# Kernel optimization log

Measured on AMD Instinct MI355X. Metric: run time of the kernel, lower is better.

Reference implementation:

```python
import jax, jax.numpy as jnp
import numpy as np

B, H, L, C, KD, NS = 4, 1024, 8192, 1, 64, 8  # batch, d_model, seq_len, channels, kernel_dim, num_scales
DECAY_MIN, DECAY_MAX = 1.0, 4.0


def _interp_linear(x, scale):
    """F.interpolate(mode='linear', align_corners=False) for integer scale on last axis."""
    if scale == 1:
        return x
    Lin = x.shape[-1]
    Lout = Lin * scale
    pos = (jnp.arange(Lout, dtype=x.dtype) + 0.5) / scale - 0.5
    lo = jnp.floor(pos)
    w = pos - lo  # fractional weight toward hi
    lo_i = jnp.clip(lo.astype(jnp.int32), 0, Lin - 1)
    hi_i = jnp.clip(lo.astype(jnp.int32) + 1, 0, Lin - 1)
    return x[..., lo_i] * (1.0 - w) + x[..., hi_i] * w


def setup_inputs() -> dict:
    key = jax.random.key(0)
    k1, k2, k3, k4 = jax.random.split(key, 4)
    return {
        "u": jax.random.normal(k1, (B, H, L), jnp.float32),
        "kernels": jax.random.normal(k2, (NS, C, H, KD), jnp.float32),
        "D": jax.random.normal(k3, (C, H), jnp.float32),
        "W_out": jax.random.normal(k4, (H, C * H), jnp.float32) / np.sqrt(C * H).astype(np.float32),
        "b_out": jnp.zeros((H,), jnp.float32),
    }


def reference(u, kernels, D, W_out, b_out):
    # --- multi-scale kernel synthesis ('cat' mode, init_scale=0) ---
    mult = jnp.linspace(DECAY_MIN, DECAY_MAX, H).astype(u.dtype).reshape(1, H, 1)
    parts = [
        _interp_linear(kernels[i], 2 ** max(0, i - 1)) * mult ** (NS - 1 - i)
        for i in range(NS)
    ]
    k = jnp.concatenate(parts, axis=-1)  # (C, H, 8192) == (C, H, L) for these dims
    # kernel_norm is computed from the untruncated kernel and detached (buffer)
    knorm = jax.lax.stop_gradient(jnp.linalg.norm(k, axis=-1, keepdims=True))  # (C, H, 1)
    k = k[..., :L] / knorm

    # --- FFT long convolution (causal, via 2L-padded circular conv) ---
    n = 2 * L
    k_f = jnp.fft.rfft(k, n=n)                 # (C, H, L+1) complex
    u_f = jnp.fft.rfft(u, n=n)                 # (B, H, L+1) complex
    y = jnp.fft.irfft(u_f[:, None, :, :] * k_f[None, :, :, :], n=n)[..., :L]  # (B, C, H, L)
    y = y + jnp.einsum('bhl,ch->bchl', u, D)   # skip connection
    y = y.reshape(u.shape[0], C * H, L)        # (B, C*H, L)

    # --- activation + output linear (1x1 conv) ---
    y = jax.nn.gelu(y, approximate=False)      # torch nn.GELU is exact erf form
    y = jnp.einsum('oh,bhl->bol', W_out, y) + b_out[None, :, None]
    return y
```

## Files before the change

kernel.cpp:

```cpp
#include <hip/hip_runtime.h>
#include <hip/hip_bf16.h>

#define LFULL 8192
#define HDIM 1024
#define KPAD 8448

typedef __attribute__((ext_vector_type(8))) short bf16x8;
typedef __attribute__((ext_vector_type(4))) float f32x4;
typedef __attribute__((ext_vector_type(16))) float f32x16;

union U16 {
  uint4 u;
  bf16x8 s;
  ushort e[8];
};

__device__ __forceinline__ ushort f2bf(float x) {
  union { float f; uint u; } a;
  a.f = x;
  uint r = a.u + 0x7fffu + ((a.u >> 16) & 1u);
  return (ushort)(r >> 16);
}
__device__ __forceinline__ float bf2f(ushort x) {
  union { uint u; float f; } a;
  a.u = ((uint)x) << 16;
  return a.f;
}

__device__ __forceinline__ void gload16(const void* src, void* lds) {
  __builtin_amdgcn_global_load_lds(
      (const __attribute__((address_space(1))) unsigned int*)src,
      (__attribute__((address_space(3))) unsigned int*)lds, 16, 0, 0);
}

__device__ __forceinline__ uint ALIGNB(uint hi, uint lo, uint sh) {
#if __has_builtin(__builtin_amdgcn_alignbyte)
  return __builtin_amdgcn_alignbyte(hi, lo, sh);
#else
  return (uint)((((unsigned long long)hi << 32) | (unsigned long long)lo) >> (8u * sh));
#endif
}

#define USWZ16(cI) ((cI) ^ (((cI) >> 4) & 15))

__global__ __launch_bounds__(256) void k_synth_kernel(
    const float* __restrict__ kern, ushort* __restrict__ kout) {
  const int h = blockIdx.x;
  const int tid = threadIdx.x;
  __shared__ float Kw[8][64];
  __shared__ __align__(16) float kv[LFULL];
  __shared__ float red[8];
  for (int idx = tid; idx < 8 * 64; idx += 256) {
    int i = idx >> 6, j = idx & 63;
    Kw[i][j] = kern[(i * HDIM + h) * 64 + j];
  }
  __syncthreads();
  const float mult = (float)(1.0 + 3.0 * (double)h / 1023.0);
  float pw[8];
  pw[7] = 1.0f;
#pragma unroll
  for (int i = 6; i >= 0; --i) pw[i] = pw[i + 1] * mult;
  float ss = 0.0f;
  for (int m = tid; m < LFULL; m += 256) {
    const int i = (m < 64) ? 0 : (32 - __clz(m >> 6));
    const int slog = (i == 0) ? 0 : (i - 1);
    const float inv_s = 1.0f / (float)(1 << slog);
    const int off = (i == 0) ? 0 : (64 << (i - 1));
    const int t = m - off;
    const float pos = ((float)t + 0.5f) * inv_s - 0.5f;
    const float lof = floorf(pos);
    const float wgt = pos - lof;
    int lo = (int)lof;
    int hi = lo + 1;
    lo = min(63, max(0, lo));
    hi = min(63, max(0, hi));
    const float val = (Kw[i][lo] * (1.0f - wgt) + Kw[i][hi] * wgt) * pw[i];
    kv[m] = val;
    ss += val * val;
  }
#pragma unroll
  for (int o = 32; o > 0; o >>= 1) ss += __shfl_xor(ss, o, 64);
  if ((tid & 63) == 0) red[tid >> 6] = ss;
  __syncthreads();
  if (tid == 0) red[0] = sqrtf(red[0] + red[1] + red[2] + red[3]);
  __syncthreads();
  const float inv_norm = 1.0f / red[0];
  ushort* krow = kout + (size_t)h * KPAD;
  for (int m = tid; m < LFULL; m += 256) krow[8191 - m] = f2bf(kv[m] * inv_norm);
  if (tid < 256) krow[8192 + tid] = 0;
}

__global__ __launch_bounds__(256, 2) void conv_mfma_kernel(
    const float* __restrict__ u, const ushort* __restrict__ kbrev,
    const float* __restrict__ Dp, ushort* __restrict__ g) {
  __shared__ __align__(16) ushort Us[4 * LFULL];
  __shared__ __align__(16) ushort Ring[4][1152];
  const int tid = threadIdx.x;
  const int h = blockIdx.x;
  const int w = tid >> 6;
  const int lane = tid & 63;
  const int c32 = lane & 31;
  const int qh = lane >> 5;
  uint4* Us4 = (uint4*)Us;

  for (int cc = tid; cc < 4096; cc += 256) {
    const int row = cc >> 10, cI = cc & 1023;
    const float* up = u + (((size_t)(row * HDIM + h)) << 13) + (cI << 3);
    const float4 v0 = *(const float4*)up;
    const float4 v1 = *(const float4*)(up + 4);
    U16 pk;
    pk.e[0] = f2bf(v0.x); pk.e[1] = f2bf(v0.y);
    pk.e[2] = f2bf(v0.z); pk.e[3] = f2bf(v0.w);
    pk.e[4] = f2bf(v1.x); pk.e[5] = f2bf(v1.y);
    pk.e[6] = f2bf(v1.z); pk.e[7] = f2bf(v1.w);
    Us4[(row << 10) + USWZ16(cI)] = pk.u;
  }

  const ushort* kr = kbrev + (size_t)h * KPAD;
  char* ringb = (char*)Ring[w];
  {
    const uint kc65 = *(const uint*)(kr + 65 * 128 + 2 * lane);
    const uint kc64 = *(const uint*)(kr + 64 * 128 + 2 * lane);
    const uint kc63 = *(const uint*)(kr + 63 * 128 + 2 * lane);
    *(uint*)(ringb + 1 * 256 + 4 * lane) = kc65;
    *(uint*)(ringb + 0 * 256 + 4 * lane) = kc64;
    *(uint*)(ringb + 2048 + 4 * lane) = kc64;
    *(uint*)(ringb + 7 * 256 + 4 * lane) = kc63;
  }
  uint kreg = *(const uint*)(kr + 62 * 128 + 2 * lane);
  __syncthreads();

  f32x16 acc[2][4];
#pragma unroll
  for (int f = 0; f < 2; ++f)
#pragma unroll
    for (int rg = 0; rg < 4; ++rg)
#pragma unroll
      for (int q = 0; q < 16; ++q) acc[f][rg][q] = 0.0f;

  const int PBASE = 8191 - c32 + 8 * qh;
  const bool s8 = ((PBASE >> 1) & 1) != 0;
  const uint sh = 2u * (uint)(PBASE & 1);

  uint4 WA[15], WB[15];

#define BUILD_W(DD, MM, DST) {                                          \
    const int P = PBASE + 128 - 128 * (DD) - 16 * (MM);                 \
    const int LL = (2 * (P & 1023)) & ~7;                               \
    const uint2 r0 = *(const uint2*)(ringb + LL);                       \
    const uint2 r1 = *(const uint2*)(ringb + LL + 8);                   \
    const uint2 r2 = *(const uint2*)(ringb + LL + 16);                  \
    const uint v0 = s8 ? r0.y : r0.x;                                   \
    const uint v1 = s8 ? r1.x : r0.y;                                   \
    const uint v2 = s8 ? r1.y : r1.x;                                   \
    const uint v3 = s8 ? r2.x : r1.y;                                   \
    const uint v4 = s8 ? r2.y : r2.x;                                   \
    (DST).x = ALIGNB(v1, v0, sh);                                       \
    (DST).y = ALIGNB(v2, v1, sh);                                       \
    (DST).z = ALIGNB(v3, v2, sh);                                       \
    (DST).w = ALIGNB(v4, v3, sh); }

#define WGET(Wc, Wf, MM) ((MM) >= 7 ? (Wf)[(MM)] : (Wc)[(MM) + 8])

#define FPART(DD, F, DIAG, Wc, Wf) {                                    \
    const int j0 = (F) * 32 + c32 - (DD);                               \
    const int jc = j0 < 0 ? 0 : j0;                                     \
    const uint zmask = ((DIAG) && (j0 < 0)) ? 0u : 0xffffffffu;         \
    _Pragma("unroll")                                                   \
    for (int ks = 0; ks < 8; ++ks) {                                    \
      const int cI = 16 * jc + 2 * ks + qh;                             \
      U16 bb;                                                           \
      bb.u = Us4[(w << 10) + USWZ16(cI)];                               \
      if (DIAG) {                                                       \
        bb.u.x &= zmask; bb.u.y &= zmask;                               \
        bb.u.z &= zmask; bb.u.w &= zmask;                               \
      }                                                                 \
      U16 a0, a1, a2, a3;                                               \
      a0.u = WGET(Wc, Wf, 8 - ks);                                      \
      a1.u = WGET(Wc, Wf, 10 - ks);                                     \
      a2.u = WGET(Wc, Wf, 12 - ks);                                     \
      a3.u = WGET(Wc, Wf, 14 - ks);                                     \
      acc[F][0] = __builtin_amdgcn_mfma_f32_32x32x16_bf16(a0.s, bb.s, acc[F][0], 0, 0, 0); \
      acc[F][1] = __builtin_amdgcn_mfma_f32_32x32x16_bf16(a1.s, bb.s, acc[F][1], 0, 0, 0); \
      acc[F][2] = __builtin_amdgcn_mfma_f32_32x32x16_bf16(a2.s, bb.s, acc[F][2], 0, 0, 0); \
      acc[F][3] = __builtin_amdgcn_mfma_f32_32x32x16_bf16(a3.s, bb.s, acc[F][3], 0, 0, 0); \
    } }

#define CONV_STEP(DD, Wc, Wf, HASF0) {                                  \
    _Pragma("unroll")                                                   \
    for (int mm = 7; mm <= 14; ++mm) BUILD_W(DD, mm, (Wf)[mm]);         \
    {                                                                   \
      const int cw0 = 62 - (DD);                                        \
      const int cw = cw0 < 0 ? 0 : cw0;                                 \
      const int sl = (cw & 7) * 256;                                    \
      *(uint*)(ringb + sl + 4 * lane) = kreg;                           \
      *(uint*)(ringb + ((sl == 0) ? 2048 : sl) + 4 * lane) = kreg;      \
      const int cn0 = 61 - (DD);                                        \
      const int cn = cn0 < 0 ? 0 : cn0;                                 \
      kreg = *(const uint*)(kr + cn * 128 + 2 * lane);                  \
    }                                                                   \
    if (HASF0) {                                                        \
      FPART(DD, 0, true, Wc, Wf);                                       \
      FPART(DD, 1, false, Wc, Wf);                                      \
    } else {                                                            \
      FPART(DD, 1, true, Wc, Wf);                                       \
    } }

#pragma unroll
  for (int mm = 1; mm <= 6; ++mm) BUILD_W(0, mm, WB[mm + 8]);

  for (int dd = 0; dd < 32; dd += 2) {
    CONV_STEP(dd, WB, WA, true);
    CONV_STEP(dd + 1, WA, WB, true);
  }
  for (int dd = 32; dd < 64; dd += 2) {
    CONV_STEP(dd, WB, WA, false);
    CONV_STEP(dd + 1, WA, WB, false);
  }

  const float Dh = Dp[h];
  ushort* gp = g + (((size_t)(w * HDIM + h)) << 13);
#pragma unroll
  for (int f = 0; f < 2; ++f) {
#pragma unroll
    for (int rg = 0; rg < 4; ++rg) {
      const int lbase = (f * 32 + c32) * 128 + rg * 32 + 4 * qh;
#pragma unroll
      for (int rq = 0; rq < 4; ++rq) {
        const int l = lbase + 8 * rq;
        const int cI = l >> 3;
        const int phys = USWZ16(cI);
        const uint2 uv = *(const uint2*)(Us + (w << 13) + (phys << 3) + 4 * qh);
        float uu[4];
        uu[0] = bf2f((ushort)(uv.x & 0xffff));
        uu[1] = bf2f((ushort)(uv.x >> 16));
        uu[2] = bf2f((ushort)(uv.y & 0xffff));
        uu[3] = bf2f((ushort)(uv.y >> 16));
        ushort o[4];
#pragma unroll
        for (int jj = 0; jj < 4; ++jj) {
          const float y = acc[f][rg][rq * 4 + jj] + Dh * uu[jj];
          const float ge = 0.5f * y * (1.0f + erff(y * 0.70710678118654752f));
          o[jj] = f2bf(ge);
        }
        uint2 op;
        op.x = (uint)o[0] | ((uint)o[1] << 16);
        op.y = (uint)o[2] | ((uint)o[3] << 16);
        *(uint2*)(gp + l) = op;
      }
    }
  }
}

__global__ __launch_bounds__(256) void transpose_kernel(
    const ushort* __restrict__ g, ushort* __restrict__ gt) {
  __shared__ __align__(16) ushort Ts[64 * 64];
  const int l0 = blockIdx.x * 64, hh0 = blockIdx.y * 64, b = blockIdx.z;
  const int tid = threadIdx.x;
#pragma unroll
  for (int p = 0; p < 2; ++p) {
    const int hh = (tid >> 3) + 32 * p;
    const int c8 = tid & 7;
    const uint4 v = *(const uint4*)(g + (((size_t)(b * HDIM + hh0 + hh)) << 13)
                                    + l0 + c8 * 8);
    ((uint4*)Ts)[hh * 8 + (c8 ^ ((hh >> 3) & 7))] = v;
  }
  __syncthreads();
#pragma unroll
  for (int p = 0; p < 2; ++p) {
    const int lr = (tid >> 3) + 32 * p;
    const int o8 = tid & 7;
    U16 pk;
#pragma unroll
    for (int j = 0; j < 8; ++j) {
      const int hq = o8 * 8 + j;
      pk.e[j] = Ts[hq * 64 + (((lr >> 3) ^ o8) << 3) + (lr & 7)];
    }
    ((uint4*)(gt + ((size_t)b * LFULL + l0 + lr) * HDIM + hh0))[o8] = pk.u;
  }
}

__global__ __launch_bounds__(256) void wcvt_kernel(const float* __restrict__ W,
                                                   ushort* __restrict__ Wb) {
  const int i = (blockIdx.x * 256 + threadIdx.x) * 8;
  const float4 v0 = *(const float4*)(W + i);
  const float4 v1 = *(const float4*)(W + i + 4);
  U16 pk;
  pk.e[0] = f2bf(v0.x); pk.e[1] = f2bf(v0.y);
  pk.e[2] = f2bf(v0.z); pk.e[3] = f2bf(v0.w);
  pk.e[4] = f2bf(v1.x); pk.e[5] = f2bf(v1.y);
  pk.e[6] = f2bf(v1.z); pk.e[7] = f2bf(v1.w);
  ((uint4*)Wb)[i >> 3] = pk.u;
}

__global__ __launch_bounds__(256, 2) void outmm_kernel(
    const ushort* __restrict__ Wb, const ushort* __restrict__ gt,
    const float* __restrict__ bo, float* __restrict__ out) {
  __shared__ __align__(16) ushort As[128 * 32];
  __shared__ __align__(16) ushort Bs[128 * 32];
  const int tid = threadIdx.x;
  const int l0 = blockIdx.x * 128, o0 = blockIdx.y * 128, b = blockIdx.z;
  const int w = tid >> 6, lane = tid & 63;
  const int wm = w >> 1, wn = w & 1;
  const int col = lane & 15, q = lane >> 4;
  const int srow = lane >> 2, scol = (lane & 3) * 8;
  f32x4 acc[4][4];
#pragma unroll
  for (int m = 0; m < 4; ++m)
#pragma unroll
    for (int n = 0; n < 4; ++n) acc[m][n] = (f32x4){0.f, 0.f, 0.f, 0.f};
  const ushort* gb = gt + ((size_t)b * LFULL) * HDIM;
  for (int kt = 0; kt < 32; ++kt) {
    const int k0 = kt * 32;
    const int r0 = w * 32;
#pragma unroll
    for (int ii = 0; ii < 2; ++ii) {
      const int ra = r0 + ii * 16 + srow;
      gload16(Wb + (size_t)(o0 + ra) * HDIM + k0 + scol,
              As + (r0 + ii * 16) * 32);
      gload16(gb + (size_t)(l0 + ra) * HDIM + k0 + scol,
              Bs + (r0 + ii * 16) * 32);
    }
    __syncthreads();
    bf16x8 aa[4], bb[4];
#pragma unroll
    for (int m = 0; m < 4; ++m) {
      aa[m] = ((const bf16x8*)As)[(wm * 64 + m * 16 + col) * 4 + q];
      bb[m] = ((const bf16x8*)Bs)[(wn * 64 + m * 16 + col) * 4 + q];
    }
#pragma unroll
    for (int m = 0; m < 4; ++m)
#pragma unroll
      for (int n = 0; n < 4; ++n)
        acc[m][n] = __builtin_amdgcn_mfma_f32_16x16x32_bf16(aa[m], bb[n],
                                                            acc[m][n], 0, 0, 0);
    __syncthreads();
  }
#pragma unroll
  for (int m = 0; m < 4; ++m) {
    const int ob = o0 + wm * 64 + m * 16 + q * 4;
    const float4 bv = *(const float4*)(bo + ob);
    const float bva[4] = {bv.x, bv.y, bv.z, bv.w};
#pragma unroll
    for (int n = 0; n < 4; ++n) {
      const int l = l0 + wn * 64 + n * 16 + col;
      float* op = out + (((size_t)(b * HDIM + ob)) << 13) + l;
#pragma unroll
      for (int v = 0; v < 4; ++v) op[(size_t)v << 13] = acc[m][n][v] + bva[v];
    }
  }
}

extern "C" void kernel_launch(void* const* d_in, const int* in_sizes, int n_in,
                              void* d_out, int out_size, void* d_ws,
                              size_t ws_size, hipStream_t stream) {
  const float* u = (const float*)d_in[0];
  const float* kern = (const float*)d_in[1];
  const float* D = (const float*)d_in[2];
  const float* W = (const float*)d_in[3];
  const float* bo = (const float*)d_in[4];
  float* out = (float*)d_out;

  char* ws = (char*)d_ws;
  ushort* g = (ushort*)ws;
  ushort* gt = (ushort*)(ws + ((size_t)64 << 20));
  ushort* kbrev = (ushort*)(ws + ((size_t)128 << 20));
  ushort* Wb = (ushort*)(ws + ((size_t)128 << 20));

  k_synth_kernel<<<HDIM, 256, 0, stream>>>(kern, kbrev);
  conv_mfma_kernel<<<HDIM, 256, 0, stream>>>(u, kbrev, D, g);
  wcvt_kernel<<<512, 256, 0, stream>>>(W, Wb);
  transpose_kernel<<<dim3(128, 16, 4), 256, 0, stream>>>(g, gt);
  outmm_kernel<<<dim3(64, 8, 4), 256, 0, stream>>>(Wb, gt, bo, out);
}
```

Baseline: 482.9 us.

## Split conv work across two blocks per channel with halved per-wave accumulators

The causal convolution kernel now launches two blocks per channel, each holding only two batch rows in shared memory. Within a block, two waves per batch row split the output row-groups. Accumulators drop from eight to four tiles per wave, and the Toeplitz weight fragments are built on the fly into a 4-entry rotating buffer instead of double 15-entry arrays. This cuts register and LDS pressure so three blocks can be resident per CU and grid parallelism doubles. In exchange, each block re-synthesises the kernel ring and B-operand loads are duplicated across the split waves.

```diff
diff --git a/kernel.cpp b/kernel.cpp
--- a/kernel.cpp
+++ b/kernel.cpp
@@ -90,22 +90,27 @@
   if (tid < 256) krow[8192 + tid] = 0;
 }
 
-__global__ __launch_bounds__(256, 2) void conv_mfma_kernel(
+__global__ __launch_bounds__(256, 3) void conv_mfma_kernel(
     const float* __restrict__ u, const ushort* __restrict__ kbrev,
     const float* __restrict__ Dp, ushort* __restrict__ g) {
-  __shared__ __align__(16) ushort Us[4 * LFULL];
+  __shared__ __align__(16) ushort Us[2 * LFULL];
   __shared__ __align__(16) ushort Ring[4][1152];
   const int tid = threadIdx.x;
-  const int h = blockIdx.x;
+  const int h = blockIdx.x >> 1;
+  const int bp = blockIdx.x & 1;
   const int w = tid >> 6;
+  const int bl = w >> 1;
+  const int ch = w & 1;
+  const int b = bp * 2 + bl;
   const int lane = tid & 63;
   const int c32 = lane & 31;
   const int qh = lane >> 5;
   uint4* Us4 = (uint4*)Us;
 
-  for (int cc = tid; cc < 4096; cc += 256) {
+  for (int cc = tid; cc < 2048; cc += 256) {
     const int row = cc >> 10, cI = cc & 1023;
-    const float* up = u + (((size_t)(row * HDIM + h)) << 13) + (cI << 3);
+    const float* up =
+        u + (((size_t)((bp * 2 + row) * HDIM + h)) << 13) + (cI << 3);
     const float4 v0 = *(const float4*)up;
     const float4 v1 = *(const float4*)(up + 4);
     U16 pk;
@@ -130,23 +135,23 @@
   uint kreg = *(const uint*)(kr + 62 * 128 + 2 * lane);
   __syncthreads();
 
-  f32x16 acc[2][4];
+  f32x16 acc[2][2];
 #pragma unroll
   for (int f = 0; f < 2; ++f)
 #pragma unroll
-    for (int rg = 0; rg < 4; ++rg)
+    for (int rg = 0; rg < 2; ++rg)
 #pragma unroll
       for (int q = 0; q < 16; ++q) acc[f][rg][q] = 0.0f;
 
   const int PBASE = 8191 - c32 + 8 * qh;
   const bool s8 = ((PBASE >> 1) & 1) != 0;
   const uint sh = 2u * (uint)(PBASE & 1);
-
-  uint4 WA[15], WB[15];
-
-#define BUILD_W(DD, MM, DST) {                                          \
-    const int P = PBASE + 128 - 128 * (DD) - 16 * (MM);                 \
-    const int LL = (2 * (P & 1023)) & ~7;                               \
+  int Pstep = PBASE - 64 * ch + 128;
+
+  uint4 W4[4];
+
+#define BW_P(PV, DST) {                                                 \
+    const int LL = (2 * ((PV) & 1023)) & ~7;                            \
     const uint2 r0 = *(const uint2*)(ringb + LL);                       \
     const uint2 r1 = *(const uint2*)(ringb + LL + 8);                   \
     const uint2 r2 = *(const uint2*)(ringb + LL + 16);                  \
@@ -160,77 +165,84 @@
     (DST).z = ALIGNB(v3, v2, sh);                                       \
     (DST).w = ALIGNB(v4, v3, sh); }
 
-#define WGET(Wc, Wf, MM) ((MM) >= 7 ? (Wf)[(MM)] : (Wc)[(MM) + 8])
-
-#define FPART(DD, F, DIAG, Wc, Wf) {                                    \
-    const int j0 = (F) * 32 + c32 - (DD);                               \
-    const int jc = j0 < 0 ? 0 : j0;                                     \
-    const uint zmask = ((DIAG) && (j0 < 0)) ? 0u : 0xffffffffu;         \
-    _Pragma("unroll")                                                   \
-    for (int ks = 0; ks < 8; ++ks) {                                    \
-      const int cI = 16 * jc + 2 * ks + qh;                             \
-      U16 bb;                                                           \
-      bb.u = Us4[(w << 10) + USWZ16(cI)];                               \
-      if (DIAG) {                                                       \
-        bb.u.x &= zmask; bb.u.y &= zmask;                               \
-        bb.u.z &= zmask; bb.u.w &= zmask;                               \
-      }                                                                 \
-      U16 a0, a1, a2, a3;                                               \
-      a0.u = WGET(Wc, Wf, 8 - ks);                                      \
-      a1.u = WGET(Wc, Wf, 10 - ks);                                     \
-      a2.u = WGET(Wc, Wf, 12 - ks);                                     \
-      a3.u = WGET(Wc, Wf, 14 - ks);                                     \
-      acc[F][0] = __builtin_amdgcn_mfma_f32_32x32x16_bf16(a0.s, bb.s, acc[F][0], 0, 0, 0); \
-      acc[F][1] = __builtin_amdgcn_mfma_f32_32x32x16_bf16(a1.s, bb.s, acc[F][1], 0, 0, 0); \
-      acc[F][2] = __builtin_amdgcn_mfma_f32_32x32x16_bf16(a2.s, bb.s, acc[F][2], 0, 0, 0); \
-      acc[F][3] = __builtin_amdgcn_mfma_f32_32x32x16_bf16(a3.s, bb.s, acc[F][3], 0, 0, 0); \
-    } }
-
-#define CONV_STEP(DD, Wc, Wf, HASF0) {                                  \
-    _Pragma("unroll")                                                   \
-    for (int mm = 7; mm <= 14; ++mm) BUILD_W(DD, mm, (Wf)[mm]);         \
-    {                                                                   \
-      const int cw0 = 62 - (DD);                                        \
-      const int cw = cw0 < 0 ? 0 : cw0;                                 \
-      const int sl = (cw & 7) * 256;                                    \
-      *(uint*)(ringb + sl + 4 * lane) = kreg;                           \
-      *(uint*)(ringb + ((sl == 0) ? 2048 : sl) + 4 * lane) = kreg;      \
-      const int cn0 = 61 - (DD);                                        \
-      const int cn = cn0 < 0 ? 0 : cn0;                                 \
-      kreg = *(const uint*)(kr + cn * 128 + 2 * lane);                  \
-    }                                                                   \
-    if (HASF0) {                                                        \
-      FPART(DD, 0, true, Wc, Wf);                                       \
-      FPART(DD, 1, false, Wc, Wf);                                      \
-    } else {                                                            \
-      FPART(DD, 1, true, Wc, Wf);                                       \
-    } }
-
-#pragma unroll
-  for (int mm = 1; mm <= 6; ++mm) BUILD_W(0, mm, WB[mm + 8]);
-
-  for (int dd = 0; dd < 32; dd += 2) {
-    CONV_STEP(dd, WB, WA, true);
-    CONV_STEP(dd + 1, WA, WB, true);
-  }
-  for (int dd = 32; dd < 64; dd += 2) {
-    CONV_STEP(dd, WB, WA, false);
-    CONV_STEP(dd + 1, WA, WB, false);
+#define RING_MAINT(DD) {                                                \
+    const int cw0 = 62 - (DD);                                          \
+    const int cw = cw0 < 0 ? 0 : cw0;                                   \
+    const int sl = (cw & 7) * 256;                                      \
+    *(uint*)(ringb + sl + 4 * lane) = kreg;                             \
+    *(uint*)(ringb + ((sl == 0) ? 2048 : sl) + 4 * lane) = kreg;        \
+    const int cn0 = 61 - (DD);                                          \
+    const int cn = cn0 < 0 ? 0 : cn0;                                   \
+    kreg = *(const uint*)(kr + cn * 128 + 2 * lane); }
+
+  for (int d = 0; d < 32; ++d) {
+    RING_MAINT(d);
+    const int j00 = c32 - d;
+    const int jc0 = j00 < 0 ? 0 : j00;
+    const uint mz0 = (j00 < 0) ? 0u : 0xffffffffu;
+    const int pb0 = jc0 << 4, px0 = jc0 & 15;
+    const int jc1 = 32 + c32 - d;
+    const int pb1 = jc1 << 4, px1 = jc1 & 15;
+#pragma unroll
+    for (int ks = 0; ks < 8; ++ks) {
+      const int P0 = Pstep - 128 + 16 * ks;
+      BW_P(P0, W4[ks & 3]);
+      if (ks < 2) BW_P(P0 - 32, W4[(ks + 2) & 3]);
+      const int t = 2 * ks + qh;
+      U16 b1;
+      b1.u = Us4[(bl << 10) + pb1 + (t ^ px1)];
+      acc[1][0] = __builtin_amdgcn_mfma_f32_32x32x16_bf16(
+          ((U16*)&W4[ks & 3])->s, b1.s, acc[1][0], 0, 0, 0);
+      acc[1][1] = __builtin_amdgcn_mfma_f32_32x32x16_bf16(
+          ((U16*)&W4[(ks + 2) & 3])->s, b1.s, acc[1][1], 0, 0, 0);
+      U16 b0;
+      b0.u = Us4[(bl << 10) + pb0 + (t ^ px0)];
+      b0.u.x &= mz0; b0.u.y &= mz0; b0.u.z &= mz0; b0.u.w &= mz0;
+      acc[0][0] = __builtin_amdgcn_mfma_f32_32x32x16_bf16(
+          ((U16*)&W4[ks & 3])->s, b0.s, acc[0][0], 0, 0, 0);
+      acc[0][1] = __builtin_amdgcn_mfma_f32_32x32x16_bf16(
+          ((U16*)&W4[(ks + 2) & 3])->s, b0.s, acc[0][1], 0, 0, 0);
+    }
+    Pstep -= 128;
+  }
+  for (int d = 32; d < 64; ++d) {
+    RING_MAINT(d);
+    const int j01 = 32 + c32 - d;
+    const int jc1 = j01 < 0 ? 0 : j01;
+    const uint mz1 = (j01 < 0) ? 0u : 0xffffffffu;
+    const int pb1 = jc1 << 4, px1 = jc1 & 15;
+#pragma unroll
+    for (int ks = 0; ks < 8; ++ks) {
+      const int P0 = Pstep - 128 + 16 * ks;
+      BW_P(P0, W4[ks & 3]);
+      if (ks < 2) BW_P(P0 - 32, W4[(ks + 2) & 3]);
+      const int t = 2 * ks + qh;
+      U16 b1;
+      b1.u = Us4[(bl << 10) + pb1 + (t ^ px1)];
+      b1.u.x &= mz1; b1.u.y &= mz1; b1.u.z &= mz1; b1.u.w &= mz1;
+      acc[1][0] = __builtin_amdgcn_mfma_f32_32x32x16_bf16(
+          ((U16*)&W4[ks & 3])->s, b1.s, acc[1][0], 0, 0, 0);
+      acc[1][1] = __builtin_amdgcn_mfma_f32_32x32x16_bf16(
+          ((U16*)&W4[(ks + 2) & 3])->s, b1.s, acc[1][1], 0, 0, 0);
+    }
+    Pstep -= 128;
   }
 
   const float Dh = Dp[h];
-  ushort* gp = g + (((size_t)(w * HDIM + h)) << 13);
+  ushort* gp = g + (((size_t)(b * HDIM + h)) << 13);
 #pragma unroll
   for (int f = 0; f < 2; ++f) {
 #pragma unroll
-    for (int rg = 0; rg < 4; ++rg) {
+    for (int rgl = 0; rgl < 2; ++rgl) {
+      const int rg = 2 * ch + rgl;
       const int lbase = (f * 32 + c32) * 128 + rg * 32 + 4 * qh;
 #pragma unroll
       for (int rq = 0; rq < 4; ++rq) {
         const int l = lbase + 8 * rq;
         const int cI = l >> 3;
         const int phys = USWZ16(cI);
-        const uint2 uv = *(const uint2*)(Us + (w << 13) + (phys << 3) + 4 * qh);
+        const uint2 uv =
+            *(const uint2*)(Us + (bl << 13) + (phys << 3) + 4 * qh);
         float uu[4];
         uu[0] = bf2f((ushort)(uv.x & 0xffff));
         uu[1] = bf2f((ushort)(uv.x >> 16));
@@ -239,7 +251,7 @@
         ushort o[4];
 #pragma unroll
         for (int jj = 0; jj < 4; ++jj) {
-          const float y = acc[f][rg][rq * 4 + jj] + Dh * uu[jj];
+          const float y = acc[f][rgl][rq * 4 + jj] + Dh * uu[jj];
           const float ge = 0.5f * y * (1.0f + erff(y * 0.70710678118654752f));
           o[jj] = f2bf(ge);
         }
@@ -368,7 +380,7 @@
   ushort* Wb = (ushort*)(ws + ((size_t)128 << 20));
 
   k_synth_kernel<<<HDIM, 256, 0, stream>>>(kern, kbrev);
-  conv_mfma_kernel<<<HDIM, 256, 0, stream>>>(u, kbrev, D, g);
+  conv_mfma_kernel<<<2 * HDIM, 256, 0, stream>>>(u, kbrev, D, g);
   wcvt_kernel<<<512, 256, 0, stream>>>(W, Wb);
   transpose_kernel<<<dim3(128, 16, 4), 256, 0, stream>>>(g, gt);
   outmm_kernel<<<dim3(64, 8, 4), 256, 0, stream>>>(Wb, gt, bo, out);
```

Result: slower. 544.2 us (+12.7%).

## Replace per-wave kernel ring with shared 8-phase pre-shifted ring and aligned loads

Applied to the files above, without the earlier changes.

Replaces each wave's private Toeplitz kernel ring, which needed three uint2 loads plus select and alignbyte per A-fragment, with one block-shared ring stored in 8 phase-shifted copies (even and odd halfword shifts, staggered per wave). Each lane then fetches its A-fragment with a single aligned 16-byte LDS load. The ring is shared across the four waves, so every step now ends with an lgkmcnt wait and a block barrier. The B-operand swizzle address is also simplified by hoisting the XOR terms. This cuts VALU and LDS instruction count in the inner loop, at the cost of a barrier per diagonal step.

```diff
diff --git a/kernel.cpp b/kernel.cpp
--- a/kernel.cpp
+++ b/kernel.cpp
@@ -94,7 +94,7 @@
     const float* __restrict__ u, const ushort* __restrict__ kbrev,
     const float* __restrict__ Dp, ushort* __restrict__ g) {
   __shared__ __align__(16) ushort Us[4 * LFULL];
-  __shared__ __align__(16) ushort Ring[4][1152];
+  __shared__ __align__(16) ushort RingC[8 * 512];
   const int tid = threadIdx.x;
   const int h = blockIdx.x;
   const int w = tid >> 6;
@@ -102,6 +102,7 @@
   const int c32 = lane & 31;
   const int qh = lane >> 5;
   uint4* Us4 = (uint4*)Us;
+  char* ringB = (char*)RingC;
 
   for (int cc = tid; cc < 4096; cc += 256) {
     const int row = cc >> 10, cI = cc & 1023;
@@ -117,17 +118,19 @@
   }
 
   const ushort* kr = kbrev + (size_t)h * KPAD;
-  char* ringb = (char*)Ring[w];
-  {
-    const uint kc65 = *(const uint*)(kr + 65 * 128 + 2 * lane);
-    const uint kc64 = *(const uint*)(kr + 64 * 128 + 2 * lane);
-    const uint kc63 = *(const uint*)(kr + 63 * 128 + 2 * lane);
-    *(uint*)(ringb + 1 * 256 + 4 * lane) = kc65;
-    *(uint*)(ringb + 0 * 256 + 4 * lane) = kc64;
-    *(uint*)(ringb + 2048 + 4 * lane) = kc64;
-    *(uint*)(ringb + 7 * 256 + 4 * lane) = kc63;
-  }
-  uint kreg = *(const uint*)(kr + 62 * 128 + 2 * lane);
+  char* ringE = ringB + (2 * w) * 1024;
+  char* ringO = ringB + (2 * w + 1) * 1024;
+#pragma unroll
+  for (int cn = 62; cn <= 64; ++cn) {
+    const int x0 = 128 * cn + 2 * lane;
+    const uint kEp = *(const uint*)(kr + x0);
+    const uint kMp = *(const uint*)(kr + x0 - 2);
+    const int off = (2 * x0 + 4 * w) & 1023;
+    *(uint*)(ringE + off) = kEp;
+    *(uint*)(ringO + off) = ALIGNB(kEp, kMp, 2);
+  }
+  uint kE = *(const uint*)(kr + 61 * 128 + 2 * lane);
+  uint kM = *(const uint*)(kr + 61 * 128 + 2 * lane - 2);
   __syncthreads();
 
   f32x16 acc[2][4];
@@ -139,84 +142,67 @@
       for (int q = 0; q < 16; ++q) acc[f][rg][q] = 0.0f;
 
   const int PBASE = 8191 - c32 + 8 * qh;
-  const bool s8 = ((PBASE >> 1) & 1) != 0;
-  const uint sh = 2u * (uint)(PBASE & 1);
-
-  uint4 WA[15], WB[15];
-
-#define BUILD_W(DD, MM, DST) {                                          \
-    const int P = PBASE + 128 - 128 * (DD) - 16 * (MM);                 \
-    const int LL = (2 * (P & 1023)) & ~7;                               \
-    const uint2 r0 = *(const uint2*)(ringb + LL);                       \
-    const uint2 r1 = *(const uint2*)(ringb + LL + 8);                   \
-    const uint2 r2 = *(const uint2*)(ringb + LL + 16);                  \
-    const uint v0 = s8 ? r0.y : r0.x;                                   \
-    const uint v1 = s8 ? r1.x : r0.y;                                   \
-    const uint v2 = s8 ? r1.y : r1.x;                                   \
-    const uint v3 = s8 ? r2.x : r1.y;                                   \
-    const uint v4 = s8 ? r2.y : r2.x;                                   \
-    (DST).x = ALIGNB(v1, v0, sh);                                       \
-    (DST).y = ALIGNB(v2, v1, sh);                                       \
-    (DST).z = ALIGNB(v3, v2, sh);                                       \
-    (DST).w = ALIGNB(v4, v3, sh); }
-
-#define WGET(Wc, Wf, MM) ((MM) >= 7 ? (Wf)[(MM)] : (Wc)[(MM) + 8])
-
-#define FPART(DD, F, DIAG, Wc, Wf) {                                    \
+  const int sph = (c32 + 1) & 7;
+  const char* ringR = ringB + sph * 1024;
+  int bd = 2 * (PBASE + sph) + 256;
+
+  uint4 WF[8];
+  uint4 WC[6];
+#pragma unroll
+  for (int i = 0; i < 6; ++i) WC[i] = make_uint4(0, 0, 0, 0);
+
+#define WGETX(MM) ((MM) >= 7 ? WF[(MM)-7] : WC[(MM)-1])
+
+#define FPART(DD, F, DIAG) {                                            \
     const int j0 = (F) * 32 + c32 - (DD);                               \
     const int jc = j0 < 0 ? 0 : j0;                                     \
     const uint zmask = ((DIAG) && (j0 < 0)) ? 0u : 0xffffffffu;         \
+    const int pb = jc << 4;                                             \
+    const int px = jc & 15;                                             \
     _Pragma("unroll")                                                   \
     for (int ks = 0; ks < 8; ++ks) {                                    \
-      const int cI = 16 * jc + 2 * ks + qh;                             \
+      const int t = 2 * ks + qh;                                        \
       U16 bb;                                                           \
-      bb.u = Us4[(w << 10) + USWZ16(cI)];                               \
+      bb.u = Us4[(w << 10) + pb + (t ^ px)];                            \
       if (DIAG) {                                                       \
         bb.u.x &= zmask; bb.u.y &= zmask;                               \
         bb.u.z &= zmask; bb.u.w &= zmask;                               \
       }                                                                 \
       U16 a0, a1, a2, a3;                                               \
-      a0.u = WGET(Wc, Wf, 8 - ks);                                      \
-      a1.u = WGET(Wc, Wf, 10 - ks);                                     \
-      a2.u = WGET(Wc, Wf, 12 - ks);                                     \
-      a3.u = WGET(Wc, Wf, 14 - ks);                                     \
+      a0.u = WGETX(8 - ks);  a1.u = WGETX(10 - ks);                     \
+      a2.u = WGETX(12 - ks); a3.u = WGETX(14 - ks);                     \
       acc[F][0] = __builtin_amdgcn_mfma_f32_32x32x16_bf16(a0.s, bb.s, acc[F][0], 0, 0, 0); \
       acc[F][1] = __builtin_amdgcn_mfma_f32_32x32x16_bf16(a1.s, bb.s, acc[F][1], 0, 0, 0); \
       acc[F][2] = __builtin_amdgcn_mfma_f32_32x32x16_bf16(a2.s, bb.s, acc[F][2], 0, 0, 0); \
       acc[F][3] = __builtin_amdgcn_mfma_f32_32x32x16_bf16(a3.s, bb.s, acc[F][3], 0, 0, 0); \
     } }
 
-#define CONV_STEP(DD, Wc, Wf, HASF0) {                                  \
+#define STEP(DD, HASF0) {                                               \
+    const int cw = (61 - (DD)) < 0 ? 0 : (61 - (DD));                   \
+    const int offw = (((cw & 3) << 8) + 4 * lane + 4 * w) & 1023;       \
+    *(uint*)(ringE + offw) = kE;                                        \
+    *(uint*)(ringO + offw) = ALIGNB(kE, kM, 2);                         \
+    const int cn = (60 - (DD)) < 0 ? 0 : (60 - (DD));                   \
+    const uint kE2 = *(const uint*)(kr + cn * 128 + 2 * lane);          \
+    const uint kM2 = *(const uint*)(kr + cn * 128 + 2 * lane - 2);      \
     _Pragma("unroll")                                                   \
-    for (int mm = 7; mm <= 14; ++mm) BUILD_W(DD, mm, (Wf)[mm]);         \
-    {                                                                   \
-      const int cw0 = 62 - (DD);                                        \
-      const int cw = cw0 < 0 ? 0 : cw0;                                 \
-      const int sl = (cw & 7) * 256;                                    \
-      *(uint*)(ringb + sl + 4 * lane) = kreg;                           \
-      *(uint*)(ringb + ((sl == 0) ? 2048 : sl) + 4 * lane) = kreg;      \
-      const int cn0 = 61 - (DD);                                        \
-      const int cn = cn0 < 0 ? 0 : cn0;                                 \
-      kreg = *(const uint*)(kr + cn * 128 + 2 * lane);                  \
+    for (int i = 0; i < 8; ++i) {                                       \
+      const int off = (bd - 224 - 32 * i) & 1023;                       \
+      WF[i] = *(const uint4*)(ringR + off);                             \
     }                                                                   \
-    if (HASF0) {                                                        \
-      FPART(DD, 0, true, Wc, Wf);                                       \
-      FPART(DD, 1, false, Wc, Wf);                                      \
-    } else {                                                            \
-      FPART(DD, 1, true, Wc, Wf);                                       \
-    } }
-
-#pragma unroll
-  for (int mm = 1; mm <= 6; ++mm) BUILD_W(0, mm, WB[mm + 8]);
-
-  for (int dd = 0; dd < 32; dd += 2) {
-    CONV_STEP(dd, WB, WA, true);
-    CONV_STEP(dd + 1, WA, WB, true);
-  }
-  for (int dd = 32; dd < 64; dd += 2) {
-    CONV_STEP(dd, WB, WA, false);
-    CONV_STEP(dd + 1, WA, WB, false);
-  }
+    if (HASF0) { FPART(DD, 0, true); FPART(DD, 1, false); }             \
+    else { FPART(DD, 1, true); }                                        \
+    WC[0] = WF[2]; WC[1] = WF[3]; WC[2] = WF[4];                        \
+    WC[3] = WF[5]; WC[4] = WF[6]; WC[5] = WF[7];                        \
+    kE = kE2; kM = kM2;                                                 \
+    bd -= 256;                                                          \
+    asm volatile("s_waitcnt lgkmcnt(0)" ::: "memory");                  \
+    __builtin_amdgcn_s_barrier();                                       \
+    __builtin_amdgcn_sched_barrier(0);                                  \
+  }
+
+  for (int d = 0; d < 32; ++d) { STEP(d, true); }
+  for (int d = 32; d < 64; ++d) { STEP(d, false); }
 
   const float Dh = Dp[h];
   ushort* gp = g + (((size_t)(w * HDIM + h)) << 13);
@@ -230,7 +216,8 @@
         const int l = lbase + 8 * rq;
         const int cI = l >> 3;
         const int phys = USWZ16(cI);
-        const uint2 uv = *(const uint2*)(Us + (w << 13) + (phys << 3) + 4 * qh);
+        const uint2 uv =
+            *(const uint2*)(Us + (w << 13) + (phys << 3) + 4 * qh);
         float uu[4];
         uu[0] = bf2f((ushort)(uv.x & 0xffff));
         uu[1] = bf2f((ushort)(uv.x >> 16));
```

Result: faster. 472.4 us (-2.2%).
